# Performance work log

Measured on AMD Instinct MI355X. Metric: run time of the kernel, lower is better.

## Reference

```python
import jax, jax.numpy as jnp
import numpy as np

HIDDEN = 1024
NUM_HEADS = 16
HEAD_DIM = HIDDEN // NUM_HEADS  # 64


def setup_inputs() -> dict:
    key = jax.random.key(0)
    ks = jax.random.split(key, 9)
    B, S = 2, 512
    scale = 0.02
    return {
        "x": jax.random.normal(ks[0], (B, S, HIDDEN), dtype=jnp.float32),
        "Wq": jax.random.normal(ks[1], (HIDDEN, HIDDEN), dtype=jnp.float32) * scale,
        "bq": jnp.zeros((HIDDEN,), dtype=jnp.float32),
        "Wk": jax.random.normal(ks[2], (HIDDEN, HIDDEN), dtype=jnp.float32) * scale,
        "bk": jnp.zeros((HIDDEN,), dtype=jnp.float32),
        "Wv": jax.random.normal(ks[3], (HIDDEN, HIDDEN), dtype=jnp.float32) * scale,
        "bv": jnp.zeros((HIDDEN,), dtype=jnp.float32),
        "Wo": jax.random.normal(ks[4], (HIDDEN, HIDDEN), dtype=jnp.float32) * scale,
        "bo": jnp.zeros((HIDDEN,), dtype=jnp.float32),
    }


def reference(x, Wq, bq, Wk, bk, Wv, bv, Wo, bo):
    B, S, D = x.shape
    H, hd = NUM_HEADS, HEAD_DIM
    q = x @ Wq + bq  # [B,S,D]
    k = x @ Wk + bk
    v = x @ Wv + bv
    # split_heads(query): [B,S,H,hd] -> [B,H,S,hd]
    q = q.reshape(B, S, H, hd).transpose(0, 2, 1, 3)
    # split_heads(key/value, head_num=1): view(B,-1,1,hd) -> [B,S*H,1,hd] -> [B,1,S*H,hd]
    k = k.reshape(B, S * H, 1, hd).transpose(0, 2, 1, 3)
    v = v.reshape(B, S * H, 1, hd).transpose(0, 2, 1, 3)
    # scores: [B,H,S,hd] @ [B,1,hd,S*H] -> [B,H,S,S*H]
    scores = jnp.einsum('bhsd,bukd->bhsk', q, k) / jnp.sqrt(jnp.float32(hd))
    probs = jax.nn.softmax(scores, axis=-1)
    # out: [B,H,S,S*H] @ [B,1,S*H,hd] -> [B,H,S,hd]
    out = jnp.einsum('bhsk,bukd->bhsd', probs, v)
    # faithful to source: transpose(-1,-2) then view(B,-1,hidden)
    out = jnp.swapaxes(out, -1, -2).reshape(B, -1, D)  # [B,S,D] (scrambled layout, as in source)
    return out @ Wo + bo
```

## Files before the change

kernel.cpp:

```cpp
#include <hip/hip_runtime.h>

typedef float f4 __attribute__((ext_vector_type(4)));
typedef float f32x16 __attribute__((ext_vector_type(16)));
typedef __bf16 v8bf __attribute__((ext_vector_type(8)));
typedef unsigned short u16x8 __attribute__((ext_vector_type(8)));
typedef unsigned u32x4 __attribute__((ext_vector_type(4)));

#define MFMA32(a, b, c) __builtin_amdgcn_mfma_f32_32x32x16_bf16(a, b, c, 0, 0, 0)
#define QSCALE 0.18033688011112042f

#if __has_builtin(__builtin_amdgcn_exp2f)
#define EXP2(x) __builtin_amdgcn_exp2f(x)
#else
#define EXP2(x) exp2f(x)
#endif

#define GLDS(src, dst)                                                        \
  __builtin_amdgcn_global_load_lds(                                           \
      (const __attribute__((address_space(1))) unsigned int*)(src),           \
      (__attribute__((address_space(3))) unsigned int*)(dst), 16, 0, 0)

__device__ __forceinline__ unsigned short f2bf(float f) {
  unsigned u = __builtin_bit_cast(unsigned, f);
  u += 0x7FFFu + ((u >> 16) & 1u);
  return (unsigned short)(u >> 16);
}
__device__ __forceinline__ float bf2f(unsigned short h) {
  unsigned u = ((unsigned)h) << 16;
  return __builtin_bit_cast(float, u);
}
__device__ __forceinline__ unsigned cvt_pk_bf16(float lo, float hi) {
  unsigned r;
  asm("v_cvt_pk_bf16_f32 %0, %1, %2" : "=v"(r) : "v"(lo), "v"(hi));
  return r;
}
__device__ __forceinline__ void plane32_swap(unsigned& x, unsigned& y) {
  asm("v_permlane32_swap_b32 %0, %1" : "+v"(x), "+v"(y));
}

__global__ __launch_bounds__(256) void prep(
    const float* __restrict__ Wq, const float* __restrict__ Wk,
    const float* __restrict__ Wv, const float* __restrict__ Wo,
    const float* __restrict__ x, unsigned short* __restrict__ wt,
    unsigned short* __restrict__ xbf) {
  const int id = blockIdx.x, tid = threadIdx.x;
  if (id < 1024) {
    __shared__ __align__(16) float T[64][65];
    const int n0 = (id & 15) << 6, k0 = ((id >> 4) & 15) << 6, z = id >> 8;
    const float* W = (z == 0) ? Wq : (z == 1) ? Wk : (z == 2) ? Wv : Wo;
    const float scale = (z == 0) ? QSCALE : 1.0f;
    {
      const int r = tid >> 2, c4 = (tid & 3) << 4;
      const float* src = W + (size_t)(k0 + r) * 1024 + n0 + c4;
#pragma unroll
      for (int u = 0; u < 4; ++u) {
        f4 t4 = *(const f4*)(src + (u << 2));
        T[c4 + (u << 2) + 0][r] = t4[0];
        T[c4 + (u << 2) + 1][r] = t4[1];
        T[c4 + (u << 2) + 2][r] = t4[2];
        T[c4 + (u << 2) + 3][r] = t4[3];
      }
    }
    __syncthreads();
    const int n = tid >> 2, kc = (tid & 3) << 4;
    unsigned short* dst = wt + ((size_t)z << 20) + (size_t)(n0 + n) * 1024 + k0 + kc;
    u16x8 o0, o1;
#pragma unroll
    for (int u = 0; u < 8; ++u) {
      o0[u] = f2bf(T[n][kc + u] * scale);
      o1[u] = f2bf(T[n][kc + 8 + u] * scale);
    }
    *(u16x8*)dst = o0;
    *(u16x8*)(dst + 8) = o1;
  } else {
    const int i = ((id - 1024) * 256 + tid) << 3;
    f4 a = *(const f4*)(x + i);
    f4 b = *(const f4*)(x + i + 4);
    u16x8 o;
#pragma unroll
    for (int u = 0; u < 4; ++u) {
      o[u] = f2bf(a[u]);
      o[u + 4] = f2bf(b[u]);
    }
    *(u16x8*)(xbf + i) = o;
  }
}

template <int MODE>
__device__ __forceinline__ void gemm_core(const unsigned short* __restrict__ A,
                                          const unsigned short* __restrict__ Bw,
                                          const float* __restrict__ bias,
                                          void* __restrict__ dst,
                                          float bscale = 1.0f) {
  __shared__ __align__(16) char lds[24576];
  const int tid = threadIdx.x, lane = tid & 63, w = tid >> 6;
  const int l31 = lane & 31, hi = lane >> 5;
  const int wm = w >> 1, wn = w & 1;
  const int m0 = blockIdx.y << 7, n0 = blockIdx.x << 6;

  f32x16 acc[2];
#pragma unroll
  for (int i = 0; i < 2; ++i)
#pragma unroll
    for (int r = 0; r < 16; ++r) acc[i][r] = 0.f;

  auto stage = [&](int buf, int k0) {
    char* base = lds + buf * 12288;
#pragma unroll
    for (int j = 0; j < 3; ++j) {
      const int c = w * 3 + j;
      const int t = lane & 7;
      if (c < 8) {
        const int row = c * 8 + (lane >> 3);
        const int u = t ^ (row & 7);
        const unsigned short* src =
            A + (size_t)(m0 + row + ((u >> 2) << 6)) * 1024 + k0 + ((u & 3) << 3);
        GLDS(src, base + c * 1024);
      } else {
        const int cm = c - 8;
        const int row = cm * 8 + (lane >> 3);
        const int u = t ^ (row & 7);
        const unsigned short* src =
            Bw + (size_t)(n0 + row + ((u >> 2) << 5)) * 1024 + k0 + ((u & 3) << 3);
        GLDS(src, base + 8192 + cm * 1024);
      }
    }
  };

  stage(0, 0);
  for (int ks = 0; ks < 32; ++ks) {
    const int buf = ks & 1;
    __syncthreads();
    if (ks < 31) stage(buf ^ 1, (ks + 1) * 32);
    const char* base = lds + buf * 12288;
#pragma unroll
    for (int kc = 0; kc < 2; ++kc) {
      const int ub = wn * 4 + kc * 2 + hi;
      v8bf b = *(const v8bf*)(base + 8192 + l31 * 128 + ((ub ^ (l31 & 7)) << 4));
#pragma unroll
      for (int im = 0; im < 2; ++im) {
        const int r = im * 32 + l31;
        const int ua = wm * 4 + kc * 2 + hi;
        v8bf a = *(const v8bf*)(base + r * 128 + ((ua ^ (r & 7)) << 4));
        acc[im] = MFMA32(a, b, acc[im]);
      }
    }
  }

  const int n = n0 + wn * 32 + l31;
  if (MODE == 0) {
    unsigned short* q = (unsigned short*)dst;
    const float bv = bias[n] * bscale;
    const int h = n >> 6, d = n & 63;
#pragma unroll
    for (int im = 0; im < 2; ++im)
#pragma unroll
      for (int r = 0; r < 16; ++r) {
        const int m = m0 + wm * 64 + im * 32 + (r & 3) + ((r >> 2) << 3) + (hi << 2);
        const int bb = m >> 9, s = m & 511;
        q[((size_t)((bb * 16 + h) * 512 + s) << 6) + d] = f2bf(acc[im][r] + bv);
      }
  } else if (MODE == 1) {
    unsigned short* vt = (unsigned short*)dst;
    const int bb = n >> 9, s = n & 511;
#pragma unroll
    for (int im = 0; im < 2; ++im)
#pragma unroll
      for (int r = 0; r < 16; ++r) {
        const int m = m0 + wm * 64 + im * 32 + (r & 3) + ((r >> 2) << 3) + (hi << 2);
        const float bv = bias[m];
        const int h = m >> 6, dd = m & 63;
        vt[((size_t)((bb * 16 + h) * 64 + dd) << 9) + s] = f2bf(acc[im][r] + bv);
      }
  } else {
    float* of = (float*)dst;
    const float bv = bias[n];
#pragma unroll
    for (int im = 0; im < 2; ++im)
#pragma unroll
      for (int r = 0; r < 16; ++r) {
        const int m = m0 + wm * 64 + im * 32 + (r & 3) + ((r >> 2) << 3) + (hi << 2);
        of[(size_t)m * 1024 + n] = acc[im][r] + bv;
      }
  }
}

__global__ __launch_bounds__(256) void gemm_qkv(
    const unsigned short* __restrict__ xbf, const unsigned short* __restrict__ wt,
    const float* __restrict__ bq, const float* __restrict__ bk,
    const float* __restrict__ bv,
    unsigned short* __restrict__ qbf, unsigned short* __restrict__ kbf,
    unsigned short* __restrict__ vtbf) {
  if (blockIdx.z == 0)
    gemm_core<0>(xbf, wt, bq, qbf, QSCALE);
  else if (blockIdx.z == 1)
    gemm_core<0>(xbf, wt + (1u << 20), bk, kbf, 1.0f);
  else
    gemm_core<1>(wt + (2u << 20), xbf, bv, vtbf, 1.0f);
}

__global__ __launch_bounds__(256) void gemm_out(
    const unsigned short* __restrict__ scr, const unsigned short* __restrict__ woT,
    const float* __restrict__ bo, float* __restrict__ out) {
  gemm_core<2>(scr, woT, bo, out, 1.0f);
}

__global__ __launch_bounds__(256) void attn_mfma(
    const unsigned short* __restrict__ qbf, const unsigned short* __restrict__ kbf,
    const unsigned short* __restrict__ vtbf, unsigned short* __restrict__ Ep,
    float* __restrict__ Lp) {
  __shared__ __align__(16) char smem[49152];
  const int tid = threadIdx.x, lane = tid & 63, w = tid >> 6;
  const int l31 = lane & 31, hi = lane >> 5;
  const int f = blockIdx.x;
  const int xcd = f & 7, g = f >> 3;
  const int b = xcd >> 2;
  const int u0 = ((xcd & 3) << 6) + g;
  const int h = u0 & 15, qt = (u0 >> 4) & 7, ks = u0 >> 7;
  const int qh = w & 1, kh = w >> 1;
  const int key0 = ks * 4096 + kh * 2048;

  const unsigned short* kb = kbf + ((size_t)b << 19);
  const unsigned short* vb = vtbf + ((size_t)b << 19);

  v8bf Qf[4];
  {
    const unsigned short* qg =
        qbf + ((size_t)((b * 16 + h) * 512 + qt * 64 + qh * 32 + l31) << 6) + hi * 8;
#pragma unroll
    for (int kc = 0; kc < 4; ++kc)
      Qf[kc] = __builtin_bit_cast(v8bf, *(const u16x8*)(qg + kc * 16));
  }
  __builtin_amdgcn_sched_barrier(0);
  asm volatile("s_waitcnt vmcnt(0)" ::: "memory");

  f32x16 acc0, acc1;
#pragma unroll
  for (int r = 0; r < 16; ++r) { acc0[r] = 0.f; acc1[r] = 0.f; }
  float lp = 0.f;

  auto stage = [&](int buf, int it) {
    const int c0 = key0 + it * 32;
#pragma unroll
    for (int j = 0; j < 4; ++j) {
      const int row = j * 8 + (lane >> 3);
      const int u = (lane & 7) ^ (row & 7);
      if (qh == 0) {
        const unsigned short* src = kb + ((size_t)(c0 + row) << 6) + (u << 3);
        GLDS(src, smem + (buf * 2 + kh) * 4096 + j * 1024);
      } else {
        const int hk = c0 >> 9, s0 = c0 & 511;
        const int d = row + ((u >> 2) << 5);
        const unsigned short* src =
            vb + ((size_t)(hk * 64 + d) << 9) + s0 + ((u & 3) << 3);
        GLDS(src, smem + 24576 + (buf * 2 + kh) * 4096 + j * 1024);
      }
    }
  };

  stage(0, 0);
  stage(1, 1);
  asm volatile("s_waitcnt vmcnt(4)" ::: "memory");
  __builtin_amdgcn_s_barrier();
  __builtin_amdgcn_sched_barrier(0);

  int cur = 0, nx1 = 1, nx2 = 2;
  for (int it = 0; it < 64; ++it) {
    if (it < 62) stage(nx2, it + 2);

    const char* Kt = smem + (cur * 2 + kh) * 4096;
    const char* Vt = smem + 24576 + (cur * 2 + kh) * 4096;

    f32x16 C;
#pragma unroll
    for (int r = 0; r < 16; ++r) C[r] = 0.f;
#pragma unroll
    for (int kc = 0; kc < 4; ++kc) {
      v8bf ak = *(const v8bf*)(Kt + l31 * 128 + (((kc * 2 + hi) ^ (l31 & 7)) << 4));
      C = MFMA32(ak, Qf[kc], C);
    }

    float p[16];
#pragma unroll
    for (int r = 0; r < 16; ++r) {
      p[r] = EXP2(C[r]);
      lp += p[r];
    }
    unsigned pk0 = cvt_pk_bf16(p[0], p[1]), pk1 = cvt_pk_bf16(p[2], p[3]);
    unsigned pk2 = cvt_pk_bf16(p[4], p[5]), pk3 = cvt_pk_bf16(p[6], p[7]);
    unsigned pk4 = cvt_pk_bf16(p[8], p[9]), pk5 = cvt_pk_bf16(p[10], p[11]);
    unsigned pk6 = cvt_pk_bf16(p[12], p[13]), pk7 = cvt_pk_bf16(p[14], p[15]);
    plane32_swap(pk0, pk2);
    plane32_swap(pk1, pk3);
    plane32_swap(pk4, pk6);
    plane32_swap(pk5, pk7);
    const v8bf pa0 = __builtin_bit_cast(v8bf, (u32x4){pk0, pk1, pk2, pk3});
    const v8bf pa1 = __builtin_bit_cast(v8bf, (u32x4){pk4, pk5, pk6, pk7});

#pragma unroll
    for (int half = 0; half < 2; ++half) {
      v8bf bv0 = *(const v8bf*)(Vt + l31 * 128 + (((half * 4 + hi) ^ (l31 & 7)) << 4));
      v8bf bv1 = *(const v8bf*)(Vt + l31 * 128 + (((half * 4 + 2 + hi) ^ (l31 & 7)) << 4));
      if (half == 0) {
        acc0 = MFMA32(pa0, bv0, acc0);
        acc0 = MFMA32(pa1, bv1, acc0);
      } else {
        acc1 = MFMA32(pa0, bv0, acc1);
        acc1 = MFMA32(pa1, bv1, acc1);
      }
    }

    if (it < 63) {
      if (it < 62)
        asm volatile("s_waitcnt vmcnt(4)" ::: "memory");
      else
        asm volatile("s_waitcnt vmcnt(0)" ::: "memory");
      __builtin_amdgcn_s_barrier();
      __builtin_amdgcn_sched_barrier(0);
    }
    const int t = cur; cur = nx1; nx1 = nx2; nx2 = t;
  }

  lp += __shfl_xor(lp, 32);

  __syncthreads();
  float* Ef = (float*)smem;
  float* Lf = (float*)(smem + 34816);
#pragma unroll
  for (int r = 0; r < 16; ++r) {
    const int q = qh * 32 + (r & 3) + ((r >> 2) << 3) + (hi << 2);
    Ef[(kh * 64 + l31) * 68 + q] = acc0[r];
    Ef[(kh * 64 + l31 + 32) * 68 + q] = acc1[r];
  }
  if (hi == 0) Lf[kh * 64 + qh * 32 + l31] = lp;
  __syncthreads();

  const size_t pb = (size_t)(((b * 16 + h) * 8 + qt) * 2 + ks);
  {
    const int q = tid >> 2, dch = (tid & 3) << 4;
    u16x8 o0, o1;
#pragma unroll
    for (int u = 0; u < 8; ++u) {
      o0[u] = f2bf(Ef[(dch + u) * 68 + q] + Ef[(64 + dch + u) * 68 + q]);
      o1[u] = f2bf(Ef[(dch + 8 + u) * 68 + q] + Ef[(64 + dch + 8 + u) * 68 + q]);
    }
    unsigned short* ep = Ep + (pb << 12) + (q << 6) + dch;
    *(u16x8*)ep = o0;
    *(u16x8*)(ep + 8) = o1;
  }
  if (tid < 64) Lp[(pb << 6) + tid] = Lf[tid] + Lf[64 + tid];
}

__global__ __launch_bounds__(256) void merge_k(const unsigned short* __restrict__ Ep,
                                               const float* __restrict__ Lp,
                                               unsigned short* __restrict__ scr) {
  const int tid = threadIdx.x;
  const int qt = blockIdx.x, h = blockIdx.y, b = blockIdx.z;
  const size_t eb = (size_t)(((b * 16 + h) * 8 + qt) * 2);
  const int d = tid & 63, qc = (tid >> 6) << 4;
  u16x8 o0, o1;
#pragma unroll
  for (int j = 0; j < 16; ++j) {
    const int q = qc + j;
    const float e = bf2f(Ep[(eb << 12) + (q << 6) + d]) +
                    bf2f(Ep[((eb + 1) << 12) + (q << 6) + d]);
    const float l = Lp[(eb << 6) + q] + Lp[((eb + 1) << 6) + q];
    const unsigned short v = f2bf(e / l);
    if (j < 8) o0[j] = v; else o1[j - 8] = v;
  }
  unsigned short* dst = scr + ((size_t)((b * 16 + h) * 64 + d) << 9) + qt * 64 + qc;
  *(u16x8*)dst = o0;
  *(u16x8*)(dst + 8) = o1;
}

extern "C" void kernel_launch(void* const* d_in, const int* in_sizes, int n_in,
                              void* d_out, int out_size, void* d_ws, size_t ws_size,
                              hipStream_t stream) {
  const float* x  = (const float*)d_in[0];
  const float* Wq = (const float*)d_in[1];
  const float* bq = (const float*)d_in[2];
  const float* Wk = (const float*)d_in[3];
  const float* bk = (const float*)d_in[4];
  const float* Wv = (const float*)d_in[5];
  const float* bv = (const float*)d_in[6];
  const float* Wo = (const float*)d_in[7];
  const float* bo = (const float*)d_in[8];
  float* out = (float*)d_out;

  char* wsb = (char*)d_ws;
  unsigned short* xbf  = (unsigned short*)wsb;
  unsigned short* scr  = (unsigned short*)wsb;
  unsigned short* qbf  = (unsigned short*)(wsb + (2u << 20));
  unsigned short* kbf  = (unsigned short*)(wsb + (4u << 20));
  unsigned short* vtbf = (unsigned short*)(wsb + (6u << 20));
  unsigned short* wt   = (unsigned short*)(wsb + (8u << 20));
  unsigned short* Ep   = (unsigned short*)(wsb + (8u << 20));
  float*          Lp   = (float*)(wsb + (12u << 20));
  unsigned short* woT  = wt + (3u << 20);

  prep<<<dim3(1536), 256, 0, stream>>>(Wq, Wk, Wv, Wo, x, wt, xbf);
  gemm_qkv<<<dim3(16, 8, 3), 256, 0, stream>>>(xbf, wt, bq, bk, bv, qbf, kbf, vtbf);
  attn_mfma<<<dim3(512), 256, 0, stream>>>(qbf, kbf, vtbf, Ep, Lp);
  merge_k<<<dim3(8, 16, 2), 256, 0, stream>>>(Ep, Lp, scr);
  gemm_out<<<dim3(16, 8), 256, 0, stream>>>(scr, woT, bo, out);
}
```

Baseline: 180.0 us.

## Split attention keys three ways across 768 blocks and merge three partials

Changes the attention split-K from 2 to 3 key splits, so 768 blocks run instead of 512, with uneven 43/42-chunk ranges per wave pair. Staging now uses pointer increments instead of recomputing addresses, and the row-sum uses four partial accumulators to shorten the dependency chain. The merge kernel sums three partials, and workspace offsets move so Lp and scr do not collide. The goal is better CU occupancy on MI355X (256 CUs) at the cost of extra partial-output traffic and dropping the XCD-aware block mapping.

```diff
diff --git a/kernel.cpp b/kernel.cpp
--- a/kernel.cpp
+++ b/kernel.cpp
@@ -212,13 +212,14 @@
   __shared__ __align__(16) char smem[49152];
   const int tid = threadIdx.x, lane = tid & 63, w = tid >> 6;
   const int l31 = lane & 31, hi = lane >> 5;
-  const int f = blockIdx.x;
-  const int xcd = f & 7, g = f >> 3;
-  const int b = xcd >> 2;
-  const int u0 = ((xcd & 3) << 6) + g;
-  const int h = u0 & 15, qt = (u0 >> 4) & 7, ks = u0 >> 7;
+  int t = blockIdx.x;
+  const int ks = t % 3; t /= 3;
+  const int qt = t & 7, h = (t >> 3) & 15, b = t >> 7;
   const int qh = w & 1, kh = w >> 1;
-  const int key0 = ks * 4096 + kh * 2048;
+
+  const int s_id = ks * 2 + kh;
+  const int chunk0 = (s_id < 4) ? 43 * s_id : 172 + 42 * (s_id - 4);
+  const int nit = (ks < 2) ? 43 : 42;
 
   const unsigned short* kb = kbf + ((size_t)b << 19);
   const unsigned short* vb = vtbf + ((size_t)b << 19);
@@ -237,36 +238,44 @@
   f32x16 acc0, acc1;
 #pragma unroll
   for (int r = 0; r < 16; ++r) { acc0[r] = 0.f; acc1[r] = 0.f; }
-  float lp = 0.f;
-
-  auto stage = [&](int buf, int it) {
-    const int c0 = key0 + it * 32;
-#pragma unroll
-    for (int j = 0; j < 4; ++j) {
-      const int row = j * 8 + (lane >> 3);
-      const int u = (lane & 7) ^ (row & 7);
-      if (qh == 0) {
-        const unsigned short* src = kb + ((size_t)(c0 + row) << 6) + (u << 3);
-        GLDS(src, smem + (buf * 2 + kh) * 4096 + j * 1024);
-      } else {
-        const int hk = c0 >> 9, s0 = c0 & 511;
-        const int d = row + ((u >> 2) << 5);
-        const unsigned short* src =
-            vb + ((size_t)(hk * 64 + d) << 9) + s0 + ((u & 3) << 3);
-        GLDS(src, smem + 24576 + (buf * 2 + kh) * 4096 + j * 1024);
-      }
+  float lps[4] = {0.f, 0.f, 0.f, 0.f};
+
+  const int r3 = lane >> 3, t7 = lane & 7;
+  const int uu = t7 ^ r3;
+  const char* sp;
+  int scnt = chunk0;
+  if (qh == 0) {
+    sp = (const char*)kb + (size_t)chunk0 * 4096 + r3 * 128 + (uu << 4);
+  } else {
+    const int c0 = chunk0 * 32;
+    const size_t uni = (size_t)(c0 >> 9) * 65536 + (size_t)(c0 & 511) * 2;
+    sp = (const char*)vb + uni + ((r3 + ((uu >> 2) << 5)) << 10) + ((uu & 3) << 4);
+  }
+
+  auto stage = [&](int buf) {
+    if (qh == 0) {
+      char* ldsb = smem + (buf * 2 + kh) * 4096;
+#pragma unroll
+      for (int j = 0; j < 4; ++j) GLDS(sp + j * 1024, ldsb + j * 1024);
+      sp += 4096;
+    } else {
+      char* ldsb = smem + 24576 + (buf * 2 + kh) * 4096;
+#pragma unroll
+      for (int j = 0; j < 4; ++j) GLDS(sp + j * 8192, ldsb + j * 1024);
+      ++scnt;
+      sp += ((scnt & 15) == 0) ? 64576 : 64;
     }
   };
 
-  stage(0, 0);
-  stage(1, 1);
+  stage(0);
+  stage(1);
   asm volatile("s_waitcnt vmcnt(4)" ::: "memory");
   __builtin_amdgcn_s_barrier();
   __builtin_amdgcn_sched_barrier(0);
 
   int cur = 0, nx1 = 1, nx2 = 2;
-  for (int it = 0; it < 64; ++it) {
-    if (it < 62) stage(nx2, it + 2);
+  for (int it = 0; it < nit; ++it) {
+    if (it < nit - 2) stage(nx2);
 
     const char* Kt = smem + (cur * 2 + kh) * 4096;
     const char* Vt = smem + 24576 + (cur * 2 + kh) * 4096;
@@ -284,7 +293,7 @@
 #pragma unroll
     for (int r = 0; r < 16; ++r) {
       p[r] = EXP2(C[r]);
-      lp += p[r];
+      lps[r >> 2] += p[r];
     }
     unsigned pk0 = cvt_pk_bf16(p[0], p[1]), pk1 = cvt_pk_bf16(p[2], p[3]);
     unsigned pk2 = cvt_pk_bf16(p[4], p[5]), pk3 = cvt_pk_bf16(p[6], p[7]);
@@ -310,17 +319,18 @@
       }
     }
 
-    if (it < 63) {
-      if (it < 62)
+    if (it < nit - 1) {
+      if (it < nit - 2)
         asm volatile("s_waitcnt vmcnt(4)" ::: "memory");
       else
         asm volatile("s_waitcnt vmcnt(0)" ::: "memory");
       __builtin_amdgcn_s_barrier();
       __builtin_amdgcn_sched_barrier(0);
     }
-    const int t = cur; cur = nx1; nx1 = nx2; nx2 = t;
-  }
-
+    const int tt = cur; cur = nx1; nx1 = nx2; nx2 = tt;
+  }
+
+  float lp = (lps[0] + lps[1]) + (lps[2] + lps[3]);
   lp += __shfl_xor(lp, 32);
 
   __syncthreads();
@@ -335,7 +345,7 @@
   if (hi == 0) Lf[kh * 64 + qh * 32 + l31] = lp;
   __syncthreads();
 
-  const size_t pb = (size_t)(((b * 16 + h) * 8 + qt) * 2 + ks);
+  const size_t pb = (size_t)(((b * 16 + h) * 8 + qt) * 3 + ks);
   {
     const int q = tid >> 2, dch = (tid & 3) << 4;
     u16x8 o0, o1;
@@ -356,15 +366,18 @@
                                                unsigned short* __restrict__ scr) {
   const int tid = threadIdx.x;
   const int qt = blockIdx.x, h = blockIdx.y, b = blockIdx.z;
-  const size_t eb = (size_t)(((b * 16 + h) * 8 + qt) * 2);
+  const size_t eb = (size_t)(((b * 16 + h) * 8 + qt) * 3);
   const int d = tid & 63, qc = (tid >> 6) << 4;
   u16x8 o0, o1;
 #pragma unroll
   for (int j = 0; j < 16; ++j) {
     const int q = qc + j;
-    const float e = bf2f(Ep[(eb << 12) + (q << 6) + d]) +
-                    bf2f(Ep[((eb + 1) << 12) + (q << 6) + d]);
-    const float l = Lp[(eb << 6) + q] + Lp[((eb + 1) << 6) + q];
+    float e = 0.f, l = 0.f;
+#pragma unroll
+    for (int i = 0; i < 3; ++i) {
+      e += bf2f(Ep[((eb + i) << 12) + (q << 6) + d]);
+      l += Lp[((eb + i) << 6) + q];
+    }
     const unsigned short v = f2bf(e / l);
     if (j < 8) o0[j] = v; else o1[j - 8] = v;
   }
@@ -389,18 +402,18 @@
 
   char* wsb = (char*)d_ws;
   unsigned short* xbf  = (unsigned short*)wsb;
-  unsigned short* scr  = (unsigned short*)wsb;
+  float*          Lp   = (float*)wsb;
   unsigned short* qbf  = (unsigned short*)(wsb + (2u << 20));
+  unsigned short* scr  = (unsigned short*)(wsb + (2u << 20));
   unsigned short* kbf  = (unsigned short*)(wsb + (4u << 20));
   unsigned short* vtbf = (unsigned short*)(wsb + (6u << 20));
   unsigned short* wt   = (unsigned short*)(wsb + (8u << 20));
   unsigned short* Ep   = (unsigned short*)(wsb + (8u << 20));
-  float*          Lp   = (float*)(wsb + (12u << 20));
   unsigned short* woT  = wt + (3u << 20);
 
   prep<<<dim3(1536), 256, 0, stream>>>(Wq, Wk, Wv, Wo, x, wt, xbf);
   gemm_qkv<<<dim3(16, 8, 3), 256, 0, stream>>>(xbf, wt, bq, bk, bv, qbf, kbf, vtbf);
-  attn_mfma<<<dim3(512), 256, 0, stream>>>(qbf, kbf, vtbf, Ep, Lp);
+  attn_mfma<<<dim3(768), 256, 0, stream>>>(qbf, kbf, vtbf, Ep, Lp);
   merge_k<<<dim3(8, 16, 2), 256, 0, stream>>>(Ep, Lp, scr);
   gemm_out<<<dim3(16, 8), 256, 0, stream>>>(scr, woT, bo, out);
 }
```

After: 173.3 us. 1.04x faster.
